# Optimization experiments

Measured on AMD Instinct MI355X. Metric: run time of the kernel, lower is better.

## Reference

```python
import jax, jax.numpy as jnp
import numpy as np

N = 8192
DIM_IN = 1024
DIM_INNER = 1024
DIM_OUT = 1024


def setup_inputs() -> dict:
    key = jax.random.key(0)
    k1, k2, k3, k4 = jax.random.split(key, 4)
    x = jax.random.normal(k1, (N, DIM_IN), dtype=jnp.float32)
    # torch nn.Linear weights, stored transposed for right-multiplication
    Wqkv = jax.random.normal(k2, (DIM_IN, 3 * DIM_INNER), dtype=jnp.float32) * (DIM_IN ** -0.5)
    Wout = jax.random.normal(k3, (DIM_INNER, DIM_OUT), dtype=jnp.float32) * (DIM_INNER ** -0.5)
    bout = jax.random.normal(k4, (DIM_OUT,), dtype=jnp.float32) * 0.01
    return {"x": x, "Wqkv": Wqkv, "Wout": Wout, "bout": bout}


def reference(x, Wqkv, Wout, bout):
    scale = DIM_INNER ** -0.5
    qkv = x @ Wqkv                      # [N, 3*Di]
    q, k, v = jnp.split(qkv, 3, axis=-1)  # each [N, Di]
    sim = jnp.einsum('id,jd->ij', q, k) * scale  # [N, N]
    # causal mask: future positions (j > i) filled with -finfo.max
    i = jnp.arange(sim.shape[0])[:, None]
    j = jnp.arange(sim.shape[1])[None, :]
    sim = jnp.where(j > i, -jnp.finfo(sim.dtype).max, sim)
    attn = jax.nn.softmax(sim, axis=-1)
    out = jnp.einsum('ij,jd->id', attn, v)  # [N, Di]
    return out @ Wout + bout            # [N, Do]
```

## Files before the change

### kernel.cpp

```cpp
#include <hip/hip_runtime.h>
#include <hip/hip_bf16.h>


typedef __bf16 v8bf __attribute__((ext_vector_type(8)));
typedef float  v4f  __attribute__((ext_vector_type(4)));

struct __align__(8) S4 { short x, y, z, w; };

__device__ inline short f2bf(float f) {
  __hip_bfloat16 h = __float2bfloat16(f);
  return *reinterpret_cast<short*>(&h);
}
__device__ inline float bf2f(short s) {
  unsigned u = ((unsigned)(unsigned short)s) << 16;
  float f;
  __builtin_memcpy(&f, &u, 4);
  return f;
}

__device__ inline void stage_tile(const short* gbase, int ldg, short* lds, int tid) {
#pragma unroll
  for (int p = 0; p < 2; ++p) {
    const int c = p * 256 + tid;
    const v8bf val = *(const v8bf*)(gbase + (size_t)(c >> 2) * ldg + (c & 3) * 8);
    *(v8bf*)(lds + c * 8) = val;
  }
}

__device__ inline void mma_step(const short* As, const short* Bs, v4f acc[4][4],
                                int lane, int wm, int wn) {
  const int qd = lane >> 4, r16 = lane & 15;
  const short* ab = As + (wm * 64 + r16) * 32 + qd * 8;
  const short* bb = Bs + (wn * 64 + r16) * 32 + qd * 8;
  v8bf a[4], b[4];
#pragma unroll
  for (int t = 0; t < 4; ++t) {
    a[t] = *(const v8bf*)(ab + t * 512);
    b[t] = *(const v8bf*)(bb + t * 512);
  }
#pragma unroll
  for (int mt = 0; mt < 4; ++mt)
#pragma unroll
    for (int nt = 0; nt < 4; ++nt)
      acc[mt][nt] = __builtin_amdgcn_mfma_f32_16x16x32_bf16(a[mt], b[nt], acc[mt][nt], 0, 0, 0);
}

#define ACC_INIT(acc)                              \
  _Pragma("unroll") for (int i_ = 0; i_ < 4; ++i_) \
  _Pragma("unroll") for (int j_ = 0; j_ < 4; ++j_) \
      acc[i_][j_] = (v4f){0.f, 0.f, 0.f, 0.f};

__global__ __launch_bounds__(256) void k_zerof(float* __restrict__ p, int n) {
  const int i = blockIdx.x * 256 + threadIdx.x;
  if (i < n) p[i] = 0.f;
}

__global__ __launch_bounds__(256) void k_detect(const unsigned short* __restrict__ xs,
                                                int* __restrict__ flag) {
  __shared__ int cnt;
  if (threadIdx.x == 0) cnt = 0;
  __syncthreads();
  int local = 0;
  for (int i = threadIdx.x; i < 4096; i += 256) {
    const unsigned e = (xs[i] >> 7) & 0xFFu;
    if (e >= 0xC0u) ++local;
  }
  if (local) atomicAdd(&cnt, local);
  __syncthreads();
  if (threadIdx.x == 0) *flag = (cnt > 8) ? 1 : 0;
}

__global__ __launch_bounds__(256) void k_convert(const void* __restrict__ in,
                                                 short* __restrict__ out, int n,
                                                 const int* __restrict__ flag) {
  const int stride = gridDim.x * blockDim.x;
  int i = blockIdx.x * blockDim.x + threadIdx.x;
  if (*flag != 0) {
    const float* p = (const float*)in;
    for (; i < n; i += stride) out[i] = f2bf(p[i]);
  } else {
    const short* p = (const short*)in;
    for (; i < n; i += stride) out[i] = p[i];
  }
}

__global__ __launch_bounds__(256) void k_to_f32(const void* __restrict__ in,
                                                float* __restrict__ out, int n,
                                                const int* __restrict__ flag) {
  const int stride = gridDim.x * blockDim.x;
  int i = blockIdx.x * blockDim.x + threadIdx.x;
  if (*flag != 0) {
    const float* p = (const float*)in;
    for (; i < n; i += stride) out[i] = p[i];
  } else {
    const short* p = (const short*)in;
    for (; i < n; i += stride) out[i] = bf2f(p[i]);
  }
}

__global__ __launch_bounds__(256) void k_convT(const void* __restrict__ in,
                                               short* __restrict__ out, int R, int C,
                                               const int* __restrict__ flag) {
  __shared__ short t[32][33];
  const int xx = threadIdx.x & 31, y0 = threadIdx.x >> 5;
  const int c0 = blockIdx.x * 32, r0 = blockIdx.y * 32;
  if (*flag != 0) {
    const float* p = (const float*)in;
#pragma unroll
    for (int i = 0; i < 4; ++i) {
      int r = y0 + i * 8;
      t[r][xx] = f2bf(p[(size_t)(r0 + r) * C + c0 + xx]);
    }
  } else {
    const short* p = (const short*)in;
#pragma unroll
    for (int i = 0; i < 4; ++i) {
      int r = y0 + i * 8;
      t[r][xx] = p[(size_t)(r0 + r) * C + c0 + xx];
    }
  }
  __syncthreads();
#pragma unroll
  for (int i = 0; i < 4; ++i) {
    int r = y0 + i * 8;
    out[(size_t)(c0 + r) * R + r0 + xx] = t[xx][r];
  }
}

__global__ __launch_bounds__(256) void k_gemm_qkv(const short* __restrict__ x,
                                                  const short* __restrict__ wt,
                                                  short* __restrict__ qk,
                                                  short* __restrict__ vT) {
  __shared__ short As[4096], Bs[4096];
  const int tid = threadIdx.x, lane = tid & 63, wave = tid >> 6;
  const int wm = wave >> 1, wn = wave & 1;
  const int m0 = blockIdx.x * 128, n0 = blockIdx.y * 128;
  v4f acc[4][4];
  ACC_INIT(acc)
  for (int k0 = 0; k0 < 1024; k0 += 32) {
    __syncthreads();
    stage_tile(x + (size_t)m0 * 1024 + k0, 1024, As, tid);
    stage_tile(wt + (size_t)n0 * 1024 + k0, 1024, Bs, tid);
    __syncthreads();
    mma_step(As, Bs, acc, lane, wm, wn);
  }
  const int qd = lane >> 4, c16 = lane & 15;
#pragma unroll
  for (int mt = 0; mt < 4; ++mt) {
    const int rl = wm * 64 + mt * 16 + qd * 4;
#pragma unroll
    for (int nt = 0; nt < 4; ++nt) {
      const int cl = wn * 64 + nt * 16 + c16;
      const int n = n0 + cl;
      if (n < 2048) {
#pragma unroll
        for (int r = 0; r < 4; ++r)
          qk[(size_t)(m0 + rl + r) * 2048 + n] = f2bf(acc[mt][nt][r]);
      } else {
        S4 p;
        p.x = f2bf(acc[mt][nt][0]);
        p.y = f2bf(acc[mt][nt][1]);
        p.z = f2bf(acc[mt][nt][2]);
        p.w = f2bf(acc[mt][nt][3]);
        *reinterpret_cast<S4*>(vT + (size_t)(n - 2048) * 8192 + (m0 + rl)) = p;
      }
    }
  }
}

__global__ __launch_bounds__(256) void k_qk_exp(const short* __restrict__ qk,
                                                short* __restrict__ E,
                                                float* __restrict__ l) {
  __shared__ short As[4096], Bs[4096];
  __shared__ float srow[128][2];
  const int tid = threadIdx.x, lane = tid & 63, wave = tid >> 6;
  const int wm = wave >> 1, wn = wave & 1;
  const int b = (int)blockIdx.x;
  int I = (int)((sqrtf(8.f * (float)b + 1.f) - 1.f) * 0.5f);
  while ((I + 1) * (I + 2) / 2 <= b) ++I;
  while (I * (I + 1) / 2 > b) --I;
  const int J = b - I * (I + 1) / 2;
  const int m0 = I * 128, n0 = J * 128;
  v4f acc[4][4];
  ACC_INIT(acc)
  for (int k0 = 0; k0 < 1024; k0 += 32) {
    __syncthreads();
    stage_tile(qk + (size_t)m0 * 2048 + k0, 2048, As, tid);
    stage_tile(qk + 1024 + (size_t)n0 * 2048 + k0, 2048, Bs, tid);
    __syncthreads();
    mma_step(As, Bs, acc, lane, wm, wn);
  }
  short* tb = E + (size_t)(I * (I + 1) / 2 + J) * 16384;
  const int qd = lane >> 4, c16 = lane & 15;
  float rp[4][4];
#pragma unroll
  for (int mt = 0; mt < 4; ++mt)
#pragma unroll
    for (int r = 0; r < 4; ++r) rp[mt][r] = 0.f;
#pragma unroll
  for (int mt = 0; mt < 4; ++mt) {
    const int rl = wm * 64 + mt * 16 + qd * 4;
#pragma unroll
    for (int nt = 0; nt < 4; ++nt) {
      const int cl = wn * 64 + nt * 16 + c16;
      const int gj = n0 + cl;
#pragma unroll
      for (int r = 0; r < 4; ++r) {
        const int gi = m0 + rl + r;
        const float s = fminf(acc[mt][nt][r] * 0.03125f, 60.f);
        const float e = (gj > gi) ? 0.f : __expf(s);
        tb[(rl + r) * 128 + cl] = f2bf(e);
        rp[mt][r] += e;
      }
    }
  }
#pragma unroll
  for (int mt = 0; mt < 4; ++mt)
#pragma unroll
    for (int r = 0; r < 4; ++r) {
      float v = rp[mt][r];
      v += __shfl_xor(v, 1);
      v += __shfl_xor(v, 2);
      v += __shfl_xor(v, 4);
      v += __shfl_xor(v, 8);
      rp[mt][r] = v;
    }
  if ((lane & 15) == 0) {
#pragma unroll
    for (int mt = 0; mt < 4; ++mt)
#pragma unroll
      for (int r = 0; r < 4; ++r)
        srow[wm * 64 + mt * 16 + qd * 4 + r][wn] = rp[mt][r];
  }
  __syncthreads();
  if (tid < 128) atomicAdd(&l[m0 + tid], srow[tid][0] + srow[tid][1]);
}

__global__ __launch_bounds__(256) void k_pv(const short* __restrict__ E,
                                            const short* __restrict__ vT,
                                            const float* __restrict__ l,
                                            short* __restrict__ attn) {
  __shared__ short As[4096], Bs[2048];
  const int tid = threadIdx.x, lane = tid & 63, wave = tid >> 6;
  const int wm = wave >> 1, wn = wave & 1;
  const int bx = (int)blockIdx.x;
  const int n0 = (int)blockIdx.y * 64;
  const int qd = lane >> 4, r16 = lane & 15;
  for (int half = 0; half < 2; ++half) {
    const int I = half ? 63 - bx : bx;
    const int m0 = I * 128;
    const size_t rowbase = (size_t)(I * (I + 1) / 2) * 16384;
    v4f acc[4][2];
#pragma unroll
    for (int mt = 0; mt < 4; ++mt)
#pragma unroll
      for (int nt = 0; nt < 2; ++nt) acc[mt][nt] = (v4f){0.f, 0.f, 0.f, 0.f};
    const int nch = (I + 1) * 4;
    for (int t = 0; t < nch; ++t) {
      const int J = t >> 2, jj = t & 3;
      __syncthreads();
      stage_tile(E + rowbase + (size_t)J * 16384 + jj * 32, 128, As, tid);
      {
        const short* g = vT + (size_t)(n0 + (tid >> 2)) * 8192 + (size_t)J * 128 + jj * 32 + (tid & 3) * 8;
        *(v8bf*)(Bs + tid * 8) = *(const v8bf*)g;
      }
      __syncthreads();
      const short* ab = As + (wm * 64 + r16) * 32 + qd * 8;
      const short* bb = Bs + (wn * 32 + r16) * 32 + qd * 8;
      v8bf a[4], b[2];
#pragma unroll
      for (int u = 0; u < 4; ++u) a[u] = *(const v8bf*)(ab + u * 512);
#pragma unroll
      for (int u = 0; u < 2; ++u) b[u] = *(const v8bf*)(bb + u * 512);
#pragma unroll
      for (int mt = 0; mt < 4; ++mt)
#pragma unroll
        for (int nt = 0; nt < 2; ++nt)
          acc[mt][nt] = __builtin_amdgcn_mfma_f32_16x16x32_bf16(a[mt], b[nt], acc[mt][nt], 0, 0, 0);
    }
    const int c16 = lane & 15;
#pragma unroll
    for (int mt = 0; mt < 4; ++mt) {
      const int rl = wm * 64 + mt * 16 + qd * 4;
      float inv[4];
#pragma unroll
      for (int r = 0; r < 4; ++r) inv[r] = 1.0f / fmaxf(l[m0 + rl + r], 1e-30f);
#pragma unroll
      for (int nt = 0; nt < 2; ++nt) {
        const int cl = wn * 32 + nt * 16 + c16;
#pragma unroll
        for (int r = 0; r < 4; ++r)
          attn[(size_t)(m0 + rl + r) * 1024 + n0 + cl] = f2bf(acc[mt][nt][r] * inv[r]);
      }
    }
    __syncthreads();
  }
}

__global__ __launch_bounds__(256) void k_gemm_out(const short* __restrict__ attn,
                                                  const short* __restrict__ wt,
                                                  const float* __restrict__ bout,
                                                  float* __restrict__ out) {
  __shared__ short As[4096], Bs[4096];
  const int tid = threadIdx.x, lane = tid & 63, wave = tid >> 6;
  const int wm = wave >> 1, wn = wave & 1;
  const int m0 = blockIdx.x * 128, n0 = blockIdx.y * 128;
  v4f acc[4][4];
  ACC_INIT(acc)
  for (int k0 = 0; k0 < 1024; k0 += 32) {
    __syncthreads();
    stage_tile(attn + (size_t)m0 * 1024 + k0, 1024, As, tid);
    stage_tile(wt + (size_t)n0 * 1024 + k0, 1024, Bs, tid);
    __syncthreads();
    mma_step(As, Bs, acc, lane, wm, wn);
  }
  const int qd = lane >> 4, c16 = lane & 15;
#pragma unroll
  for (int mt = 0; mt < 4; ++mt) {
    const int rl = wm * 64 + mt * 16 + qd * 4;
#pragma unroll
    for (int nt = 0; nt < 4; ++nt) {
      const int cl = wn * 64 + nt * 16 + c16;
      const float bias = bout[n0 + cl];
#pragma unroll
      for (int r = 0; r < 4; ++r)
        out[(size_t)(m0 + rl + r) * 1024 + n0 + cl] = acc[mt][nt][r] + bias;
    }
  }
}

extern "C" void kernel_launch(void* const* d_in, const int* in_sizes, int n_in,
                              void* d_out, int out_size, void* d_ws, size_t ws_size,
                              hipStream_t stream) {
  (void)out_size; (void)ws_size;
  const void *x = d_in[0], *Wqkv = d_in[1], *Wout = d_in[2], *bout = d_in[3];
  for (int i = 0; i < n_in; ++i) {
    switch (in_sizes[i]) {
      case 8192 * 1024: x = d_in[i]; break;
      case 1024 * 3072: Wqkv = d_in[i]; break;
      case 1024 * 1024: Wout = d_in[i]; break;
      case 1024:        bout = d_in[i]; break;
      default: break;
    }
  }

  char* ws = (char*)d_ws;
  short* qk    = (short*)(ws);
  short* vT    = (short*)(ws + 33554432);
  short* E     = (short*)(ws + 50331648);
  short* xb    = (short*)(ws + 118489088);
  short* attn  = xb;
  short* WqT   = (short*)(ws + 135266304);
  short* WoT   = (short*)(ws + 141557760);
  float* boutf = (float*)(ws + 143654912);
  float* lsum  = (float*)(ws + 143659008);
  int*   flag  = (int*)  (ws + 143691776);

  k_detect<<<1, 256, 0, stream>>>((const unsigned short*)x, flag);
  k_zerof<<<32, 256, 0, stream>>>(lsum, 8192);
  k_convert<<<1024, 256, 0, stream>>>(x, xb, 8192 * 1024, flag);
  k_to_f32<<<1, 256, 0, stream>>>(bout, boutf, 1024, flag);
  k_convT<<<dim3(96, 32), 256, 0, stream>>>(Wqkv, WqT, 1024, 3072, flag);
  k_convT<<<dim3(32, 32), 256, 0, stream>>>(Wout, WoT, 1024, 1024, flag);
  k_gemm_qkv<<<dim3(64, 24), 256, 0, stream>>>(xb, WqT, qk, vT);
  k_qk_exp<<<dim3(2080), 256, 0, stream>>>(qk, E, lsum);
  k_pv<<<dim3(32, 16), 256, 0, stream>>>(E, vT, lsum, attn);
  k_gemm_out<<<dim3(64, 8), 256, 0, stream>>>(attn, WoT, boutf, (float*)d_out);
}
```

Baseline: 485.3 us.

## Prefetch full 128-wide PV chunks into registers and use direct global-to-LDS loads

The PV kernel now stages a whole 128-column K chunk of E and vT per iteration, four times larger than before. It prefetches the next chunk into registers while MFMAs run on the current LDS tile, which cuts barriers per chunk and hides global load latency. stage_tile, used by the GEMM kernels, now uses global_load_lds direct-to-LDS loads instead of going through VGPRs. The costs are more LDS per block (48KB), higher register pressure from the prefetch buffers, and possible occupancy loss.

```diff
diff --git a/kernel.cpp b/kernel.cpp
--- a/kernel.cpp
+++ b/kernel.cpp
@@ -22,8 +22,11 @@
 #pragma unroll
   for (int p = 0; p < 2; ++p) {
     const int c = p * 256 + tid;
-    const v8bf val = *(const v8bf*)(gbase + (size_t)(c >> 2) * ldg + (c & 3) * 8);
-    *(v8bf*)(lds + c * 8) = val;
+    const short* g = gbase + (size_t)(c >> 2) * ldg + (c & 3) * 8;
+    short* l = lds + p * 2048 + (tid >> 6) * 512;
+    __builtin_amdgcn_global_load_lds(
+        (__attribute__((address_space(1))) void*)(void*)g,
+        (__attribute__((address_space(3))) void*)l, 16, 0, 0);
   }
 }
 
@@ -236,11 +239,39 @@
   if (tid < 128) atomicAdd(&l[m0 + tid], srow[tid][0] + srow[tid][1]);
 }
 
+__device__ inline void pv_load(const short* __restrict__ Et, const short* __restrict__ vb,
+                               v8bf av[8], v8bf bv[4], int tid) {
+#pragma unroll
+  for (int p = 0; p < 8; ++p) {
+    const int c = p * 256 + tid;
+    av[p] = *(const v8bf*)(Et + (c >> 4) * 128 + (c & 15) * 8);
+  }
+#pragma unroll
+  for (int p = 0; p < 4; ++p) {
+    const int c = p * 256 + tid;
+    bv[p] = *(const v8bf*)(vb + (size_t)(c >> 4) * 8192 + (c & 15) * 8);
+  }
+}
+__device__ inline void pv_write(short* __restrict__ As, short* __restrict__ Bs,
+                                const v8bf av[8], const v8bf bv[4], int tid) {
+#pragma unroll
+  for (int p = 0; p < 8; ++p) {
+    const int c = p * 256 + tid, cc = c & 15;
+    *(v8bf*)(As + (cc >> 2) * 4096 + (c >> 4) * 32 + (cc & 3) * 8) = av[p];
+  }
+#pragma unroll
+  for (int p = 0; p < 4; ++p) {
+    const int c = p * 256 + tid, cc = c & 15;
+    *(v8bf*)(Bs + (cc >> 2) * 2048 + (c >> 4) * 32 + (cc & 3) * 8) = bv[p];
+  }
+}
+
 __global__ __launch_bounds__(256) void k_pv(const short* __restrict__ E,
                                             const short* __restrict__ vT,
                                             const float* __restrict__ l,
                                             short* __restrict__ attn) {
-  __shared__ short As[4096], Bs[2048];
+  __shared__ short As[16384];
+  __shared__ short Bs[8192];
   const int tid = threadIdx.x, lane = tid & 63, wave = tid >> 6;
   const int wm = wave >> 1, wn = wave & 1;
   const int bx = (int)blockIdx.x;
@@ -249,34 +280,41 @@
   for (int half = 0; half < 2; ++half) {
     const int I = half ? 63 - bx : bx;
     const int m0 = I * 128;
-    const size_t rowbase = (size_t)(I * (I + 1) / 2) * 16384;
+    const short* Erow = E + (size_t)(I * (I + 1) / 2) * 16384;
+    const short* vb = vT + (size_t)n0 * 8192;
     v4f acc[4][2];
 #pragma unroll
     for (int mt = 0; mt < 4; ++mt)
 #pragma unroll
       for (int nt = 0; nt < 2; ++nt) acc[mt][nt] = (v4f){0.f, 0.f, 0.f, 0.f};
-    const int nch = (I + 1) * 4;
-    for (int t = 0; t < nch; ++t) {
-      const int J = t >> 2, jj = t & 3;
-      __syncthreads();
-      stage_tile(E + rowbase + (size_t)J * 16384 + jj * 32, 128, As, tid);
-      {
-        const short* g = vT + (size_t)(n0 + (tid >> 2)) * 8192 + (size_t)J * 128 + jj * 32 + (tid & 3) * 8;
-        *(v8bf*)(Bs + tid * 8) = *(const v8bf*)g;
+    v8bf av[8], bv[4];
+    pv_load(Erow, vb, av, bv, tid);
+    __syncthreads();
+    pv_write(As, Bs, av, bv, tid);
+    __syncthreads();
+    for (int J = 0; J <= I; ++J) {
+      const bool more = (J < I);
+      if (more) pv_load(Erow + (size_t)(J + 1) * 16384, vb + (J + 1) * 128, av, bv, tid);
+#pragma unroll
+      for (int jj = 0; jj < 4; ++jj) {
+        const short* ab = As + jj * 4096 + (wm * 64 + r16) * 32 + qd * 8;
+        const short* bb = Bs + jj * 2048 + (wn * 32 + r16) * 32 + qd * 8;
+        v8bf a[4], b[2];
+#pragma unroll
+        for (int u = 0; u < 4; ++u) a[u] = *(const v8bf*)(ab + u * 512);
+#pragma unroll
+        for (int u = 0; u < 2; ++u) b[u] = *(const v8bf*)(bb + u * 512);
+#pragma unroll
+        for (int mt = 0; mt < 4; ++mt)
+#pragma unroll
+          for (int nt = 0; nt < 2; ++nt)
+            acc[mt][nt] = __builtin_amdgcn_mfma_f32_16x16x32_bf16(a[mt], b[nt], acc[mt][nt], 0, 0, 0);
       }
-      __syncthreads();
-      const short* ab = As + (wm * 64 + r16) * 32 + qd * 8;
-      const short* bb = Bs + (wn * 32 + r16) * 32 + qd * 8;
-      v8bf a[4], b[2];
-#pragma unroll
-      for (int u = 0; u < 4; ++u) a[u] = *(const v8bf*)(ab + u * 512);
-#pragma unroll
-      for (int u = 0; u < 2; ++u) b[u] = *(const v8bf*)(bb + u * 512);
-#pragma unroll
-      for (int mt = 0; mt < 4; ++mt)
-#pragma unroll
-        for (int nt = 0; nt < 2; ++nt)
-          acc[mt][nt] = __builtin_amdgcn_mfma_f32_16x16x32_bf16(a[mt], b[nt], acc[mt][nt], 0, 0, 0);
+      if (more) {
+        __syncthreads();
+        pv_write(As, Bs, av, bv, tid);
+        __syncthreads();
+      }
     }
     const int c16 = lane & 15;
 #pragma unroll
@@ -293,7 +331,6 @@
           attn[(size_t)(m0 + rl + r) * 1024 + n0 + cl] = f2bf(acc[mt][nt][r] * inv[r]);
       }
     }
-    __syncthreads();
   }
 }
 
```

Result: faster. 412.6 us (-15.0%).

## Use direct global-to-LDS loads and pre-swizzle V for register-only PV

Applied to the files above, without the earlier changes.

stage_tile now uses global_load_lds so tiles are copied straight into shared memory without passing through VGPRs. The QKV GEMM writes V in a fragment-ready layout, which lets the PV kernel load E and V operands directly from global memory into registers and drop its LDS staging and barriers. The aim is to cut LDS traffic, register pressure and synchronisation in every GEMM and in PV. The cost is that PV now relies on uncoalesced or cache-served global loads for E, and the direct-to-LDS path needs the wave-contiguous layout to line up exactly with the mma_step read pattern.

```diff
diff --git a/kernel.cpp b/kernel.cpp
--- a/kernel.cpp
+++ b/kernel.cpp
@@ -22,8 +22,11 @@
 #pragma unroll
   for (int p = 0; p < 2; ++p) {
     const int c = p * 256 + tid;
-    const v8bf val = *(const v8bf*)(gbase + (size_t)(c >> 2) * ldg + (c & 3) * 8);
-    *(v8bf*)(lds + c * 8) = val;
+    const short* g = gbase + (size_t)(c >> 2) * ldg + (c & 3) * 8;
+    short* l = lds + p * 2048 + (tid >> 6) * 512;
+    __builtin_amdgcn_global_load_lds(
+        (__attribute__((address_space(1))) void*)(void*)g,
+        (__attribute__((address_space(3))) void*)l, 16, 0, 0);
   }
 }
 
@@ -130,7 +133,7 @@
 __global__ __launch_bounds__(256) void k_gemm_qkv(const short* __restrict__ x,
                                                   const short* __restrict__ wt,
                                                   short* __restrict__ qk,
-                                                  short* __restrict__ vT) {
+                                                  short* __restrict__ vF) {
   __shared__ short As[4096], Bs[4096];
   const int tid = threadIdx.x, lane = tid & 63, wave = tid >> 6;
   const int wm = wave >> 1, wn = wave & 1;
@@ -157,12 +160,17 @@
         for (int r = 0; r < 4; ++r)
           qk[(size_t)(m0 + rl + r) * 2048 + n] = f2bf(acc[mt][nt][r]);
       } else {
+        const int vdim = n - 2048;
+        const int cb = vdim >> 4, r16v = vdim & 15;
+        const int t = m0 + rl;
+        const int Jt = t >> 7, jjt = (t >> 5) & 3, qdt = (t >> 3) & 3, eb = t & 7;
         S4 p;
         p.x = f2bf(acc[mt][nt][0]);
         p.y = f2bf(acc[mt][nt][1]);
         p.z = f2bf(acc[mt][nt][2]);
         p.w = f2bf(acc[mt][nt][3]);
-        *reinterpret_cast<S4*>(vT + (size_t)(n - 2048) * 8192 + (m0 + rl)) = p;
+        *reinterpret_cast<S4*>(vF + (size_t)(cb * 64 + Jt) * 2048 +
+                               (jjt * 4 + qdt) * 128 + r16v * 8 + eb) = p;
       }
     }
   }
@@ -237,46 +245,48 @@
 }
 
 __global__ __launch_bounds__(256) void k_pv(const short* __restrict__ E,
-                                            const short* __restrict__ vT,
+                                            const short* __restrict__ vF,
                                             const float* __restrict__ l,
                                             short* __restrict__ attn) {
-  __shared__ short As[4096], Bs[2048];
   const int tid = threadIdx.x, lane = tid & 63, wave = tid >> 6;
   const int wm = wave >> 1, wn = wave & 1;
   const int bx = (int)blockIdx.x;
   const int n0 = (int)blockIdx.y * 64;
   const int qd = lane >> 4, r16 = lane & 15;
+  const int cb0 = (n0 >> 4) + wn * 2;
   for (int half = 0; half < 2; ++half) {
     const int I = half ? 63 - bx : bx;
     const int m0 = I * 128;
-    const size_t rowbase = (size_t)(I * (I + 1) / 2) * 16384;
+    const short* Erow = E + (size_t)(I * (I + 1) / 2) * 16384;
+    const short* abase = Erow + (wm * 64 + r16) * 128 + qd * 8;
     v4f acc[4][2];
 #pragma unroll
     for (int mt = 0; mt < 4; ++mt)
 #pragma unroll
       for (int nt = 0; nt < 2; ++nt) acc[mt][nt] = (v4f){0.f, 0.f, 0.f, 0.f};
-    const int nch = (I + 1) * 4;
-    for (int t = 0; t < nch; ++t) {
-      const int J = t >> 2, jj = t & 3;
-      __syncthreads();
-      stage_tile(E + rowbase + (size_t)J * 16384 + jj * 32, 128, As, tid);
-      {
-        const short* g = vT + (size_t)(n0 + (tid >> 2)) * 8192 + (size_t)J * 128 + jj * 32 + (tid & 3) * 8;
-        *(v8bf*)(Bs + tid * 8) = *(const v8bf*)g;
+    for (int J = 0; J <= I; ++J) {
+      v8bf af[4][4], bf[2][4];
+      const short* at = abase + (size_t)J * 16384;
+#pragma unroll
+      for (int mt = 0; mt < 4; ++mt)
+#pragma unroll
+        for (int jj = 0; jj < 4; ++jj)
+          af[mt][jj] = *(const v8bf*)(at + mt * 2048 + jj * 32);
+#pragma unroll
+      for (int nt = 0; nt < 2; ++nt) {
+        const short* bt = vF + (size_t)((cb0 + nt) * 64 + J) * 2048 + lane * 8;
+#pragma unroll
+        for (int jj = 0; jj < 4; ++jj)
+          bf[nt][jj] = *(const v8bf*)(bt + jj * 512);
       }
-      __syncthreads();
-      const short* ab = As + (wm * 64 + r16) * 32 + qd * 8;
-      const short* bb = Bs + (wn * 32 + r16) * 32 + qd * 8;
-      v8bf a[4], b[2];
-#pragma unroll
-      for (int u = 0; u < 4; ++u) a[u] = *(const v8bf*)(ab + u * 512);
-#pragma unroll
-      for (int u = 0; u < 2; ++u) b[u] = *(const v8bf*)(bb + u * 512);
-#pragma unroll
-      for (int mt = 0; mt < 4; ++mt)
-#pragma unroll
-        for (int nt = 0; nt < 2; ++nt)
-          acc[mt][nt] = __builtin_amdgcn_mfma_f32_16x16x32_bf16(a[mt], b[nt], acc[mt][nt], 0, 0, 0);
+#pragma unroll
+      for (int jj = 0; jj < 4; ++jj)
+#pragma unroll
+        for (int mt = 0; mt < 4; ++mt)
+#pragma unroll
+          for (int nt = 0; nt < 2; ++nt)
+            acc[mt][nt] = __builtin_amdgcn_mfma_f32_16x16x32_bf16(af[mt][jj], bf[nt][jj],
+                                                                  acc[mt][nt], 0, 0, 0);
     }
     const int c16 = lane & 15;
 #pragma unroll
@@ -293,7 +303,6 @@
           attn[(size_t)(m0 + rl + r) * 1024 + n0 + cl] = f2bf(acc[mt][nt][r] * inv[r]);
       }
     }
-    __syncthreads();
   }
 }
 
@@ -346,7 +355,7 @@
 
   char* ws = (char*)d_ws;
   short* qk    = (short*)(ws);
-  short* vT    = (short*)(ws + 33554432);
+  short* vF    = (short*)(ws + 33554432);
   short* E     = (short*)(ws + 50331648);
   short* xb    = (short*)(ws + 118489088);
   short* attn  = xb;
@@ -362,8 +371,8 @@
   k_to_f32<<<1, 256, 0, stream>>>(bout, boutf, 1024, flag);
   k_convT<<<dim3(96, 32), 256, 0, stream>>>(Wqkv, WqT, 1024, 3072, flag);
   k_convT<<<dim3(32, 32), 256, 0, stream>>>(Wout, WoT, 1024, 1024, flag);
-  k_gemm_qkv<<<dim3(64, 24), 256, 0, stream>>>(xb, WqT, qk, vT);
+  k_gemm_qkv<<<dim3(64, 24), 256, 0, stream>>>(xb, WqT, qk, vF);
   k_qk_exp<<<dim3(2080), 256, 0, stream>>>(qk, E, lsum);
-  k_pv<<<dim3(32, 16), 256, 0, stream>>>(E, vT, lsum, attn);
+  k_pv<<<dim3(32, 16), 256, 0, stream>>>(E, vF, lsum, attn);
   k_gemm_out<<<dim3(64, 8), 256, 0, stream>>>(attn, WoT, boutf, (float*)d_out);
 }
```

Measured after the change: 557.0 us. +14.8%, slower.
